# Optimization experiments

Measured on AMD Instinct MI355X. Metric: run time of the kernel, lower is better.

Reference implementation:

```python
import jax, jax.numpy as jnp
import numpy as np

B, N, DIM = 2, 2048, 1024
HEADS, DH, NUM_MEM = 8, 64, 4
EPS = 1e-5


def layer_norm(x, gamma):
    mu = x.mean(-1, keepdims=True)
    var = ((x - mu) ** 2).mean(-1, keepdims=True)
    return (x - mu) * jax.lax.rsqrt(var + EPS) * gamma


def setup_inputs() -> dict:
    key = jax.random.key(0)
    ks = jax.random.split(key, 7)
    x = jax.random.normal(ks[0], (B, N, DIM), jnp.float32)
    mask = jax.random.randint(ks[1], (B, N), 0, 2) > 0
    attn_bias = jax.random.normal(ks[2], (HEADS, N, N), jnp.float32) * 0.02
    gamma = jnp.ones((DIM,), jnp.float32)
    Wq = jax.random.normal(ks[3], (DIM, HEADS * DH), jnp.float32) * (DIM ** -0.5)
    Wkv = jax.random.normal(ks[4], (DIM, 2 * DH), jnp.float32) * (DIM ** -0.5)
    mem_kv = jax.random.normal(ks[5], (2, NUM_MEM, DH), jnp.float32)
    Wout = jax.random.normal(ks[6], (HEADS * DH, DIM), jnp.float32) * ((HEADS * DH) ** -0.5)
    return dict(x=x, attn_bias=attn_bias, gamma=gamma, Wq=Wq, Wkv=Wkv,
                mem_kv=mem_kv, Wout=Wout, mask=mask)


def reference(x, attn_bias, gamma, Wq, Wkv, mem_kv, Wout, mask):
    b, n, _ = x.shape
    # norm applied to query path only; kv comes from pre-norm x (self-attention)
    xn = layer_norm(x, gamma)
    q = (xn @ Wq).reshape(b, n, HEADS, DH).transpose(0, 2, 1, 3) * (DH ** -0.5)  # b h n d
    kv = x @ Wkv  # multi-query: single shared kv head
    k, v = kv[..., :DH], kv[..., DH:]
    mk = jnp.broadcast_to(mem_kv[0], (b, NUM_MEM, DH))
    mv = jnp.broadcast_to(mem_kv[1], (b, NUM_MEM, DH))
    k = jnp.concatenate([mk, k], axis=1)  # b (m+n) d
    v = jnp.concatenate([mv, v], axis=1)
    j = n + NUM_MEM
    bias = jnp.pad(attn_bias, ((0, 0), (0, 0), (NUM_MEM, 0)))  # zero bias on mem tokens
    maskp = jnp.pad(mask, ((0, 0), (NUM_MEM, 0)), constant_values=True)
    sim = jnp.einsum('bhid,bjd->bhij', q, k) + bias
    neg = -jnp.finfo(sim.dtype).max
    sim = jnp.where(maskp[:, None, None, :], sim, neg)
    causal = jnp.triu(jnp.ones((n, j), bool), k=NUM_MEM + 1)  # mem tokens always visible
    sim = jnp.where(causal, neg, sim)
    attn = jax.nn.softmax(sim, axis=-1)
    out = jnp.einsum('bhij,bjd->bhid', attn, v)
    out = out.transpose(0, 2, 1, 3).reshape(b, n, HEADS * DH)
    return out @ Wout
```

## Files before the change

kernel.cpp:

```cpp
#include <hip/hip_runtime.h>
#include <hip/hip_bf16.h>
#include <float.h>

#define B_ 2
#define N_ 2048
#define DIM_ 1024
#define HEADS_ 8
#define DH_ 64
#define NUM_MEM_ 4
#define ROWS_ (B_ * N_)
#define QCOLS_ (HEADS_ * DH_)
#define JTOT_ (N_ + NUM_MEM_)
#define JPAD_ 2176
#define CHUNKS_PER_BH_ 77

typedef __attribute__((ext_vector_type(8))) short short8v;
typedef __attribute__((ext_vector_type(4))) float f32x4;

static __device__ __forceinline__ ushort f2b(float f) {
    __hip_bfloat16 hb = __float2bfloat16(f);
    return *(ushort*)&hb;
}
static __device__ __forceinline__ uint pk2(float a, float b) {
    return ((uint)f2b(b) << 16) | (uint)f2b(a);
}
static __device__ __forceinline__ float b2f_lo(uint u) {
    union { uint x; float f; } c; c.x = u << 16; return c.f;
}
static __device__ __forceinline__ float b2f_hi(uint u) {
    union { uint x; float f; } c; c.x = u & 0xffff0000u; return c.f;
}

static __device__ __forceinline__ void wtrans_body(const float* __restrict__ W,
                                                   ushort* __restrict__ Wt,
                                                   int K, int N, int t) {
    int n = t % N;
    int k0 = (t / N) * 8;
    ushort u[8];
    #pragma unroll
    for (int j = 0; j < 8; ++j) u[j] = f2b(W[(size_t)(k0 + j) * N + n]);
    *(int4*)(Wt + (size_t)n * K + k0) = *(int4*)u;
}

__global__ __launch_bounds__(256) void ln_prep_kernel(const float* __restrict__ x,
                                                      const float* __restrict__ gamma,
                                                      const float* __restrict__ Wq,
                                                      const float* __restrict__ Wkv,
                                                      const float* __restrict__ Wout,
                                                      const float* __restrict__ mem_kv,
                                                      const int* __restrict__ mask,
                                                      ushort* __restrict__ xb,
                                                      ushort* __restrict__ xnb,
                                                      ushort* __restrict__ Wqt,
                                                      ushort* __restrict__ Wkvt,
                                                      ushort* __restrict__ Woutt,
                                                      ushort* __restrict__ Kb,
                                                      ushort* __restrict__ Vt,
                                                      ushort* __restrict__ amask) {
    int bid0 = blockIdx.x;
    if (bid0 < ROWS_) {
        int row = bid0;
        const float4 v = ((const float4*)(x + (size_t)row * DIM_))[threadIdx.x];
        float s  = v.x + v.y + v.z + v.w;
        float s2 = v.x * v.x + v.y * v.y + v.z * v.z + v.w * v.w;
        #pragma unroll
        for (int off = 32; off > 0; off >>= 1) {
            s  += __shfl_down(s, off);
            s2 += __shfl_down(s2, off);
        }
        __shared__ float ws1[4], ws2[4];
        int lane = threadIdx.x & 63, wid = threadIdx.x >> 6;
        if (lane == 0) { ws1[wid] = s; ws2[wid] = s2; }
        __syncthreads();
        float tot  = ws1[0] + ws1[1] + ws1[2] + ws1[3];
        float tot2 = ws2[0] + ws2[1] + ws2[2] + ws2[3];
        float mu  = tot * (1.0f / DIM_);
        float var = tot2 * (1.0f / DIM_) - mu * mu;
        float rs  = rsqrtf(var + 1e-5f);
        const float4 g = ((const float4*)gamma)[threadIdx.x];
        float vv[4] = {v.x, v.y, v.z, v.w};
        float gg[4] = {g.x, g.y, g.z, g.w};
        ushort xo[4], xno[4];
        #pragma unroll
        for (int j = 0; j < 4; ++j) {
            xo[j]  = f2b(vv[j]);
            xno[j] = f2b((vv[j] - mu) * rs * gg[j]);
        }
        *(int2*)(xb  + (size_t)row * DIM_ + threadIdx.x * 4) = *(int2*)xo;
        *(int2*)(xnb + (size_t)row * DIM_ + threadIdx.x * 4) = *(int2*)xno;
        return;
    }
    int bid = bid0 - ROWS_;
    int tid = threadIdx.x;
    if (bid < 256) {
        wtrans_body(Wq, Wqt, DIM_, QCOLS_, bid * 256 + tid);
    } else if (bid < 320) {
        wtrans_body(Wkv, Wkvt, DIM_, 2 * DH_, (bid - 256) * 256 + tid);
    } else if (bid < 576) {
        wtrans_body(Wout, Woutt, QCOLS_, DIM_, (bid - 320) * 256 + tid);
    } else if (bid < 640) {
        int t = (bid - 576) * 256 + tid;
        int d  = t & 63;
        int ji = (t >> 6) & 127;
        int b  = t >> 13;
        int j  = (ji < NUM_MEM_) ? ji : (2048 + ji);
        float kv_ = 0.f, vv = 0.f;
        if (ji < NUM_MEM_) {
            kv_ = mem_kv[ji * DH_ + d];
            vv  = mem_kv[NUM_MEM_ * DH_ + ji * DH_ + d];
        }
        Kb[((size_t)(b * JPAD_) + j) * DH_ + d] = f2b(kv_);
        Vt[((size_t)(b * DH_) + d) * JPAD_ + j] = f2b(vv);
    } else {
        int t = (bid - 640) * 256 + tid;
        if (t < B_ * JPAD_) {
            int b = t / JPAD_;
            int j = t % JPAD_;
            float v;
            if (j < NUM_MEM_) v = 0.f;
            else if (j < JTOT_) v = mask[b * N_ + (j - NUM_MEM_)] ? 0.f : -1e30f;
            else v = -1e30f;
            amask[(size_t)b * JPAD_ + j] = f2b(v);
        }
    }
}

template<int MODE>
static __device__ __forceinline__ void gemm64_body(ushort (*As)[40], ushort (*Bs)[40],
                                                   const ushort* __restrict__ A,
                                                   const ushort* __restrict__ Bt,
                                                   void* __restrict__ C,
                                                   void* __restrict__ C2,
                                                   int N, int K, int bx, int by) {
    int tid = threadIdx.x;
    int w = tid >> 6, l = tid & 63, lg = l >> 4, ll = l & 15;
    int r0 = by * 64, c0 = bx * 64;

    int arow = tid >> 2;
    int achk = (tid & 3) * 8;
    const ushort* Ap = A + (size_t)(r0 + arow) * K + achk;
    const ushort* Bp = Bt + (size_t)(c0 + arow) * K + achk;

    int4 a0 = *(const int4*)Ap;
    int4 b0 = *(const int4*)Bp;

    f32x4 acc[4] = {};

    int nk = K / 32;
    for (int ks = 0; ks < nk; ++ks) {
        __syncthreads();
        *(int4*)&As[arow][achk] = a0;
        *(int4*)&Bs[arow][achk] = b0;
        __syncthreads();
        int kn = (ks + 1 < nk) ? (ks + 1) * 32 : 0;
        a0 = *(const int4*)(Ap + kn);
        b0 = *(const int4*)(Bp + kn);
        short8v af, bf[4];
        af = *(const short8v*)&As[w * 16 + ll][lg * 8];
        #pragma unroll
        for (int ct = 0; ct < 4; ++ct)
            bf[ct] = *(const short8v*)&Bs[ct * 16 + ll][lg * 8];
        __builtin_amdgcn_s_setprio(1);
        #pragma unroll
        for (int ct = 0; ct < 4; ++ct)
            acc[ct] = __builtin_amdgcn_mfma_f32_16x16x32_bf16(af, bf[ct], acc[ct], 0, 0, 0);
        __builtin_amdgcn_s_setprio(0);
    }

    #pragma unroll
    for (int ct = 0; ct < 4; ++ct) {
        #pragma unroll
        for (int r = 0; r < 4; ++r) {
            int row = r0 + w * 16 + lg * 4 + r;
            int col = c0 + ct * 16 + ll;
            float val = acc[ct][r];
            if (MODE == 0) {
                ((ushort*)C)[(size_t)row * QCOLS_ + col] = f2b(val * 0.125f);
            } else {
                int b = row >> 11;
                int j = (row & 2047) + NUM_MEM_;
                if (col < DH_)
                    ((ushort*)C)[((size_t)(b * JPAD_) + j) * DH_ + col] = f2b(val);
                else
                    ((ushort*)C2)[((size_t)(b * DH_) + (col - DH_)) * JPAD_ + j] = f2b(val);
            }
        }
    }
}

__global__ __launch_bounds__(256) void gemm01_kernel(const ushort* __restrict__ xnb,
                                                     const ushort* __restrict__ Wqt,
                                                     ushort* __restrict__ qb,
                                                     const ushort* __restrict__ xb,
                                                     const ushort* __restrict__ Wkvt,
                                                     ushort* __restrict__ Kb,
                                                     ushort* __restrict__ Vt) {
    __shared__ ushort As[64][40];
    __shared__ ushort Bs[64][40];
    int bid = blockIdx.x;
    if (bid < 512) {
        gemm64_body<0>(As, Bs, xnb, Wqt, qb, nullptr, QCOLS_, DIM_, bid & 7, bid >> 3);
    } else {
        int r = bid - 512;
        gemm64_body<1>(As, Bs, xb, Wkvt, Kb, Vt, 2 * DH_, DIM_, r & 1, r >> 1);
    }
}

__global__ __launch_bounds__(256) void gemm_out_kernel(const ushort* __restrict__ A,
                                                       const ushort* __restrict__ Bt,
                                                       float* __restrict__ C,
                                                       int M, int N, int K) {
    __shared__ ushort As[128][40];
    __shared__ ushort Bs[64][40];
    int tid = threadIdx.x;
    int w = tid >> 6, l = tid & 63, lg = l >> 4, ll = l & 15;
    int r0 = blockIdx.y * 128, c0 = blockIdx.x * 64;

    int arow = tid >> 2;
    int achk = (tid & 3) * 8;
    const ushort* Ap  = A + (size_t)(r0 + arow) * K + achk;
    const ushort* Ap2 = Ap + (size_t)64 * K;
    const ushort* Bp  = Bt + (size_t)(c0 + arow) * K + achk;

    int4 a0 = *(const int4*)Ap;
    int4 a1 = *(const int4*)Ap2;
    int4 b0 = *(const int4*)Bp;

    f32x4 acc[2][4] = {};

    int nk = K / 32;
    for (int ks = 0; ks < nk; ++ks) {
        __syncthreads();
        *(int4*)&As[arow][achk]      = a0;
        *(int4*)&As[arow + 64][achk] = a1;
        *(int4*)&Bs[arow][achk]      = b0;
        __syncthreads();
        int kn = (ks + 1 < nk) ? (ks + 1) * 32 : 0;
        a0 = *(const int4*)(Ap + kn);
        a1 = *(const int4*)(Ap2 + kn);
        b0 = *(const int4*)(Bp + kn);
        short8v af[2], bf[4];
        af[0] = *(const short8v*)&As[w * 32 + ll][lg * 8];
        af[1] = *(const short8v*)&As[w * 32 + 16 + ll][lg * 8];
        #pragma unroll
        for (int ct = 0; ct < 4; ++ct)
            bf[ct] = *(const short8v*)&Bs[ct * 16 + ll][lg * 8];
        __builtin_amdgcn_s_setprio(1);
        #pragma unroll
        for (int rt = 0; rt < 2; ++rt)
            #pragma unroll
            for (int ct = 0; ct < 4; ++ct)
                acc[rt][ct] = __builtin_amdgcn_mfma_f32_16x16x32_bf16(af[rt], bf[ct], acc[rt][ct], 0, 0, 0);
        __builtin_amdgcn_s_setprio(0);
    }

    #pragma unroll
    for (int rt = 0; rt < 2; ++rt)
        #pragma unroll
        for (int ct = 0; ct < 4; ++ct)
            #pragma unroll
            for (int r = 0; r < 4; ++r) {
                int row = r0 + w * 32 + rt * 16 + lg * 4 + r;
                int col = c0 + ct * 16 + ll;
                C[(size_t)row * DIM_ + col] = acc[rt][ct][r];
            }
}

__global__ __launch_bounds__(256, 4) void fattn_split_kernel(const ushort* __restrict__ qb,
                                                             const ushort* __restrict__ Kb,
                                                             const ushort* __restrict__ Vt,
                                                             const float* __restrict__ bias,
                                                             const ushort* __restrict__ amask,
                                                             ushort* __restrict__ part_O,
                                                             float* __restrict__ part_ml) {
    __shared__ ushort Ks[64][72];
    __shared__ ushort Vs[64][72];
    __shared__ ushort Bb[64][68];

    int cid = blockIdx.x;
    int bh  = cid / CHUNKS_PER_BH_;
    int rem = cid - bh * CHUNKS_PER_BH_;
    int b = bh >> 3, h = bh & 7;
    int qt = 0, ci = 0;
    {
        int cum = 0;
        #pragma unroll 1
        for (int t = 0; t < 32; ++t) {
            int c = (t + 10) / 9;
            if (rem < cum + c) { qt = t; ci = rem - cum; break; }
            cum += c;
        }
    }
    int nt = qt + 2;
    int nc = (qt + 10) / 9;
    int t0 = ci * nt / nc;
    int t1 = (ci + 1) * nt / nc;
    int q0 = qt * 64;

    int tid = threadIdx.x;
    int w  = tid >> 6;
    int l  = tid & 63;
    int lg = l >> 4;
    int ll = l & 15;
    int i_row = q0 + w * 16 + ll;

    short8v aq0, aq1;
    {
        const ushort* qp = qb + ((size_t)(b * N_ + i_row)) * QCOLS_ + h * DH_;
        aq0 = *(const short8v*)(qp + lg * 8);
        aq1 = *(const short8v*)(qp + 32 + lg * 8);
    }

    int trow = tid >> 5;
    int tpc  = tid & 31;
    const float*  bias_rb = bias + ((size_t)h * N_ + q0 + trow) * N_;
    const ushort* am_row  = amask + (size_t)b * JPAD_;

    int sr = tid >> 3, sc = (tid & 7) * 8;
    const ushort* KbB = Kb + (size_t)b * JPAD_ * DH_;
    const ushort* VtB = Vt + (size_t)b * DH_ * JPAD_;

    int srcA = ((l & 16) << 1) + ll;
    int srcB = srcA + 16;
    bool hi = (l & 32) != 0;

    int jp0 = t0 * 64;
    int4 kr0 = *(const int4*)(KbB + (size_t)(jp0 + sr) * DH_ + sc);
    int4 kr1 = *(const int4*)(KbB + (size_t)(jp0 + sr + 32) * DH_ + sc);
    int4 vr0 = *(const int4*)(VtB + (size_t)sr * JPAD_ + jp0 + sc);
    int4 vr1 = *(const int4*)(VtB + (size_t)(sr + 32) * JPAD_ + jp0 + sc);

    uint bbc[8];
    {
        int j_e = jp0 + 2 * tpc;
        int sj  = j_e - NUM_MEM_;
        int sjc = sj < 0 ? 0 : (sj > N_ - 2 ? N_ - 2 : sj);
        uint am2 = *(const uint*)(am_row + j_e);
        float amf0 = b2f_lo(am2), amf1 = b2f_hi(am2);
        #pragma unroll
        for (int p = 0; p < 8; ++p) {
            float2 bv = *(const float2*)(bias_rb + (size_t)(8 * p) * N_ + sjc);
            int i_s = q0 + trow + 8 * p;
            float v0 = (j_e     < NUM_MEM_) ? 0.f : bv.x + amf0;
            float v1 = (j_e + 1 < NUM_MEM_) ? 0.f : bv.y + amf1;
            v0 = (j_e     <= i_s + NUM_MEM_) ? v0 : -1e30f;
            v1 = (j_e + 1 <= i_s + NUM_MEM_) ? v1 : -1e30f;
            bbc[p] = pk2(v0, v1);
        }
    }

    f32x4 oacc[4] = {};
    float mrow1 = -1e30f, lsum1 = 0.f;

    for (int jt = t0; jt < t1; ++jt) {
        __syncthreads();
        *(int4*)&Ks[sr][sc]      = kr0;
        *(int4*)&Ks[sr + 32][sc] = kr1;
        *(int4*)&Vs[sr][sc]      = vr0;
        *(int4*)&Vs[sr + 32][sc] = vr1;
        #pragma unroll
        for (int p = 0; p < 8; ++p)
            *(uint*)&Bb[trow + 8 * p][2 * tpc] = bbc[p];
        __syncthreads();

        int jn0 = (jt + 1 < t1 ? jt + 1 : jt) * 64;
        kr0 = *(const int4*)(KbB + (size_t)(jn0 + sr) * DH_ + sc);
        kr1 = *(const int4*)(KbB + (size_t)(jn0 + sr + 32) * DH_ + sc);
        vr0 = *(const int4*)(VtB + (size_t)sr * JPAD_ + jn0 + sc);
        vr1 = *(const int4*)(VtB + (size_t)(sr + 32) * JPAD_ + jn0 + sc);
        int j_e = jn0 + 2 * tpc;
        int sj  = j_e - NUM_MEM_;
        int sjc = sj < 0 ? 0 : (sj > N_ - 2 ? N_ - 2 : sj);
        uint am2n = *(const uint*)(am_row + j_e);
        float2 bvn[8];
        #pragma unroll
        for (int p = 0; p < 8; ++p)
            bvn[p] = *(const float2*)(bias_rb + (size_t)(8 * p) * N_ + sjc);

        float s[4][4];
        #pragma unroll
        for (int ct = 0; ct < 4; ++ct) {
            f32x4 acc = {};
            short8v bk0 = *(const short8v*)&Ks[ct * 16 + ll][lg * 8];
            short8v bk1 = *(const short8v*)&Ks[ct * 16 + ll][32 + lg * 8];
            __builtin_amdgcn_s_setprio(1);
            acc = __builtin_amdgcn_mfma_f32_16x16x32_bf16(bk0, aq0, acc, 0, 0, 0);
            acc = __builtin_amdgcn_mfma_f32_16x16x32_bf16(bk1, aq1, acc, 0, 0, 0);
            __builtin_amdgcn_s_setprio(0);
            uint2 ub = *(const uint2*)&Bb[w * 16 + ll][ct * 16 + lg * 4];
            s[ct][0] = acc[0] + b2f_lo(ub.x);
            s[ct][1] = acc[1] + b2f_hi(ub.x);
            s[ct][2] = acc[2] + b2f_lo(ub.y);
            s[ct][3] = acc[3] + b2f_hi(ub.y);
        }

        float m01 = fmaxf(fmaxf(s[0][0], s[0][1]), fmaxf(s[0][2], s[0][3]));
        float m23 = fmaxf(fmaxf(s[1][0], s[1][1]), fmaxf(s[1][2], s[1][3]));
        float m45 = fmaxf(fmaxf(s[2][0], s[2][1]), fmaxf(s[2][2], s[2][3]));
        float m67 = fmaxf(fmaxf(s[3][0], s[3][1]), fmaxf(s[3][2], s[3][3]));
        float m = fmaxf(fmaxf(m01, m23), fmaxf(m45, m67));
        m = fmaxf(m, __shfl_xor(m, 16));
        m = fmaxf(m, __shfl_xor(m, 32));
        float mn = fmaxf(mrow1, m);
        float scl = __expf(mrow1 - mn);
        mrow1 = mn;

        float ps = 0.f;
        #pragma unroll
        for (int ct = 0; ct < 4; ++ct)
            #pragma unroll
            for (int r = 0; r < 4; ++r) {
                float p = __expf(s[ct][r] - mn);
                s[ct][r] = p;
                ps += p;
            }
        ps += __shfl_xor(ps, 16);
        ps += __shfl_xor(ps, 32);
        lsum1 = lsum1 * scl + ps;

        uint pux[4], puy[4];
        #pragma unroll
        for (int ct = 0; ct < 4; ++ct) {
            pux[ct] = pk2(s[ct][0], s[ct][1]);
            puy[ct] = pk2(s[ct][2], s[ct][3]);
        }
        #pragma unroll
        for (int dt = 0; dt < 4; ++dt)
            #pragma unroll
            for (int r = 0; r < 4; ++r) oacc[dt][r] *= scl;

        #pragma unroll
        for (int c = 0; c < 2; ++c) {
            int cl = 2 * c, ch = 2 * c + 1;
            uint xA_l = (uint)__shfl((int)pux[cl], srcA);
            uint xA_h = (uint)__shfl((int)pux[ch], srcA);
            uint yA_l = (uint)__shfl((int)puy[cl], srcA);
            uint yA_h = (uint)__shfl((int)puy[ch], srcA);
            uint xB_l = (uint)__shfl((int)pux[cl], srcB);
            uint xB_h = (uint)__shfl((int)pux[ch], srcB);
            uint yB_l = (uint)__shfl((int)puy[cl], srcB);
            uint yB_h = (uint)__shfl((int)puy[ch], srcB);
            uint uu[4];
            uu[0] = hi ? xA_h : xA_l;
            uu[1] = hi ? yA_h : yA_l;
            uu[2] = hi ? xB_h : xB_l;
            uu[3] = hi ? yB_h : yB_l;
            short8v ptf = *(const short8v*)uu;
            __builtin_amdgcn_s_setprio(1);
            #pragma unroll
            for (int dt = 0; dt < 4; ++dt) {
                short8v bv = *(const short8v*)&Vs[dt * 16 + ll][c * 32 + lg * 8];
                oacc[dt] = __builtin_amdgcn_mfma_f32_16x16x32_bf16(bv, ptf, oacc[dt], 0, 0, 0);
            }
            __builtin_amdgcn_s_setprio(0);
        }

        {
            float amf0 = b2f_lo(am2n), amf1 = b2f_hi(am2n);
            #pragma unroll
            for (int p = 0; p < 8; ++p) {
                int i_s = q0 + trow + 8 * p;
                float v0 = (j_e     < NUM_MEM_) ? 0.f : bvn[p].x + amf0;
                float v1 = (j_e + 1 < NUM_MEM_) ? 0.f : bvn[p].y + amf1;
                v0 = (j_e     <= i_s + NUM_MEM_) ? v0 : -1e30f;
                v1 = (j_e + 1 <= i_s + NUM_MEM_) ? v1 : -1e30f;
                bbc[p] = pk2(v0, v1);
            }
        }
    }

    int slot = (bh * 32 + qt) * 4 + ci;
    ushort* po = part_O + (size_t)slot * 4096;
    #pragma unroll
    for (int dt = 0; dt < 4; ++dt) {
        uint2 pu;
        pu.x = pk2(oacc[dt][0], oacc[dt][1]);
        pu.y = pk2(oacc[dt][2], oacc[dt][3]);
        *(uint2*)&po[(w * 16 + ll) * 64 + dt * 16 + lg * 4] = pu;
    }
    if (lg == 0) {
        part_ml[(size_t)slot * 128 + (w * 16 + ll) * 2]     = mrow1;
        part_ml[(size_t)slot * 128 + (w * 16 + ll) * 2 + 1] = lsum1;
    }
}

__global__ __launch_bounds__(256) void merge_kernel(const ushort* __restrict__ part_O,
                                                    const float* __restrict__ part_ml,
                                                    ushort* __restrict__ attn_ob) {
    int bid = blockIdx.x;
    int qt = bid & 31;
    int bh = bid >> 5;
    int b = bh >> 3, h = bh & 7;
    int nc = (qt + 10) / 9;
    int tid = threadIdx.x;
    int row = tid >> 2;
    int dseg = (tid & 3) * 16;
    int slot0 = bid * 4;

    float M = -1e30f;
    #pragma unroll
    for (int c = 0; c < 4; ++c) {
        if (c >= nc) break;
        M = fmaxf(M, part_ml[(size_t)(slot0 + c) * 128 + row * 2]);
    }
    float den = 0.f;
    float num[16] = {};
    #pragma unroll
    for (int c = 0; c < 4; ++c) {
        if (c >= nc) break;
        float m_c = part_ml[(size_t)(slot0 + c) * 128 + row * 2];
        float l_c = part_ml[(size_t)(slot0 + c) * 128 + row * 2 + 1];
        float wgt = __expf(m_c - M);
        den += wgt * l_c;
        const uint4* src = (const uint4*)(part_O + (size_t)(slot0 + c) * 4096 + row * 64 + dseg);
        uint4 v0 = src[0];
        uint4 v1 = src[1];
        uint uu[8] = { v0.x, v0.y, v0.z, v0.w, v1.x, v1.y, v1.z, v1.w };
        #pragma unroll
        for (int e = 0; e < 8; ++e) {
            num[e * 2 + 0] += wgt * b2f_lo(uu[e]);
            num[e * 2 + 1] += wgt * b2f_hi(uu[e]);
        }
    }
    float inv = 1.f / den;
    ushort o[16];
    #pragma unroll
    for (int e = 0; e < 16; ++e) o[e] = f2b(num[e] * inv);
    int i = qt * 64 + row;
    ushort* dst = attn_ob + ((size_t)(b * N_ + i)) * QCOLS_ + h * DH_ + dseg;
    *(int4*)dst = *(int4*)o;
    *(int4*)(dst + 8) = *(int4*)(o + 8);
}

extern "C" void kernel_launch(void* const* d_in, const int* in_sizes, int n_in,
                              void* d_out, int out_size, void* d_ws, size_t ws_size,
                              hipStream_t stream) {
    const float* x         = (const float*)d_in[0];
    const float* attn_bias = (const float*)d_in[1];
    const float* gamma     = (const float*)d_in[2];
    const float* Wq        = (const float*)d_in[3];
    const float* Wkv       = (const float*)d_in[4];
    const float* mem_kv    = (const float*)d_in[5];
    const float* Wout      = (const float*)d_in[6];
    const int*   mask      = (const int*)d_in[7];
    float* out = (float*)d_out;

    char* wsb = (char*)d_ws;
    ushort* xb      = (ushort*)wsb;
    ushort* xnb     = (ushort*)(wsb + (8u  << 20));
    ushort* qb      = (ushort*)(wsb + (16u << 20));
    ushort* attn_ob = (ushort*)(wsb + (20u << 20));
    ushort* Kb      = (ushort*)(wsb + (24u << 20));
    ushort* Vt      = (ushort*)(wsb + (25u << 20));
    ushort* Wqt     = (ushort*)(wsb + (26u << 20));
    ushort* Wkvt    = (ushort*)(wsb + (27u << 20));
    ushort* Woutt   = (ushort*)(wsb + (28u << 20));
    ushort* amask   = (ushort*)(wsb + (29u << 20));
    ushort* part_O  = (ushort*)(wsb + (32u << 20));
    float*  part_ml = (float*)(wsb + (64u << 20));

    ln_prep_kernel<<<ROWS_ + 657, 256, 0, stream>>>(x, gamma, Wq, Wkv, Wout, mem_kv, mask,
                                                    xb, xnb, Wqt, Wkvt, Woutt, Kb, Vt, amask);
    gemm01_kernel<<<640, 256, 0, stream>>>(xnb, Wqt, qb, xb, Wkvt, Kb, Vt);
    fattn_split_kernel<<<16 * CHUNKS_PER_BH_, 256, 0, stream>>>(qb, Kb, Vt, attn_bias, amask, part_O, part_ml);
    merge_kernel<<<512, 256, 0, stream>>>(part_O, part_ml, attn_ob);
    gemm_out_kernel<<<dim3(DIM_ / 64, ROWS_ / 128), 256, 0, stream>>>(attn_ob, Woutt, out, ROWS_, DIM_, QCOLS_);
}
```

Measured before the change: 94.89 us.

## Deepen GEMM K-tiles to 64, write single-chunk attention directly, reorder blocks

Both projection GEMMs now stage 64-wide K slices per iteration instead of 32. This halves the number of barrier-separated loop steps and issues two MFMAs per fragment, at the cost of more shared memory and registers. The attention kernel now normalizes and writes the output directly for query tiles that have only one chunk, and the merge kernel skips those tiles. This removes partial-buffer traffic for them. The attention block index is also interleaved by batch so that blocks sharing the same bias head run close together.

```diff
diff --git a/kernel.cpp b/kernel.cpp
--- a/kernel.cpp
+++ b/kernel.cpp
@@ -126,7 +126,7 @@
 }
 
 template<int MODE>
-static __device__ __forceinline__ void gemm64_body(ushort (*As)[40], ushort (*Bs)[40],
+static __device__ __forceinline__ void gemm64_body(ushort (*As)[72], ushort (*Bs)[72],
                                                    const ushort* __restrict__ A,
                                                    const ushort* __restrict__ Bt,
                                                    void* __restrict__ C,
@@ -136,34 +136,47 @@
     int w = tid >> 6, l = tid & 63, lg = l >> 4, ll = l & 15;
     int r0 = by * 64, c0 = bx * 64;
 
-    int arow = tid >> 2;
-    int achk = (tid & 3) * 8;
-    const ushort* Ap = A + (size_t)(r0 + arow) * K + achk;
-    const ushort* Bp = Bt + (size_t)(c0 + arow) * K + achk;
-
-    int4 a0 = *(const int4*)Ap;
-    int4 b0 = *(const int4*)Bp;
+    int sr = tid >> 3;
+    int sc = (tid & 7) * 8;
+    const ushort* Ap0 = A + (size_t)(r0 + sr) * K + sc;
+    const ushort* Ap1 = A + (size_t)(r0 + sr + 32) * K + sc;
+    const ushort* Bp0 = Bt + (size_t)(c0 + sr) * K + sc;
+    const ushort* Bp1 = Bt + (size_t)(c0 + sr + 32) * K + sc;
+
+    int4 a0 = *(const int4*)Ap0;
+    int4 a1 = *(const int4*)Ap1;
+    int4 b0 = *(const int4*)Bp0;
+    int4 b1 = *(const int4*)Bp1;
 
     f32x4 acc[4] = {};
 
-    int nk = K / 32;
+    int nk = K / 64;
     for (int ks = 0; ks < nk; ++ks) {
         __syncthreads();
-        *(int4*)&As[arow][achk] = a0;
-        *(int4*)&Bs[arow][achk] = b0;
+        *(int4*)&As[sr][sc]      = a0;
+        *(int4*)&As[sr + 32][sc] = a1;
+        *(int4*)&Bs[sr][sc]      = b0;
+        *(int4*)&Bs[sr + 32][sc] = b1;
         __syncthreads();
-        int kn = (ks + 1 < nk) ? (ks + 1) * 32 : 0;
-        a0 = *(const int4*)(Ap + kn);
-        b0 = *(const int4*)(Bp + kn);
-        short8v af, bf[4];
-        af = *(const short8v*)&As[w * 16 + ll][lg * 8];
-        #pragma unroll
-        for (int ct = 0; ct < 4; ++ct)
-            bf[ct] = *(const short8v*)&Bs[ct * 16 + ll][lg * 8];
+        int kn = (ks + 1 < nk) ? (ks + 1) * 64 : 0;
+        a0 = *(const int4*)(Ap0 + kn);
+        a1 = *(const int4*)(Ap1 + kn);
+        b0 = *(const int4*)(Bp0 + kn);
+        b1 = *(const int4*)(Bp1 + kn);
+        short8v af0 = *(const short8v*)&As[w * 16 + ll][lg * 8];
+        short8v af1 = *(const short8v*)&As[w * 16 + ll][32 + lg * 8];
+        short8v bf0[4], bf1[4];
+        #pragma unroll
+        for (int ct = 0; ct < 4; ++ct) {
+            bf0[ct] = *(const short8v*)&Bs[ct * 16 + ll][lg * 8];
+            bf1[ct] = *(const short8v*)&Bs[ct * 16 + ll][32 + lg * 8];
+        }
         __builtin_amdgcn_s_setprio(1);
         #pragma unroll
-        for (int ct = 0; ct < 4; ++ct)
-            acc[ct] = __builtin_amdgcn_mfma_f32_16x16x32_bf16(af, bf[ct], acc[ct], 0, 0, 0);
+        for (int ct = 0; ct < 4; ++ct) {
+            acc[ct] = __builtin_amdgcn_mfma_f32_16x16x32_bf16(af0, bf0[ct], acc[ct], 0, 0, 0);
+            acc[ct] = __builtin_amdgcn_mfma_f32_16x16x32_bf16(af1, bf1[ct], acc[ct], 0, 0, 0);
+        }
         __builtin_amdgcn_s_setprio(0);
     }
 
@@ -195,8 +208,8 @@
                                                      const ushort* __restrict__ Wkvt,
                                                      ushort* __restrict__ Kb,
                                                      ushort* __restrict__ Vt) {
-    __shared__ ushort As[64][40];
-    __shared__ ushort Bs[64][40];
+    __shared__ ushort As[64][72];
+    __shared__ ushort Bs[64][72];
     int bid = blockIdx.x;
     if (bid < 512) {
         gemm64_body<0>(As, Bs, xnb, Wqt, qb, nullptr, QCOLS_, DIM_, bid & 7, bid >> 3);
@@ -210,47 +223,60 @@
                                                        const ushort* __restrict__ Bt,
                                                        float* __restrict__ C,
                                                        int M, int N, int K) {
-    __shared__ ushort As[128][40];
-    __shared__ ushort Bs[64][40];
+    __shared__ ushort As[128][72];
+    __shared__ ushort Bs[64][72];
     int tid = threadIdx.x;
     int w = tid >> 6, l = tid & 63, lg = l >> 4, ll = l & 15;
     int r0 = blockIdx.y * 128, c0 = blockIdx.x * 64;
 
-    int arow = tid >> 2;
-    int achk = (tid & 3) * 8;
-    const ushort* Ap  = A + (size_t)(r0 + arow) * K + achk;
-    const ushort* Ap2 = Ap + (size_t)64 * K;
-    const ushort* Bp  = Bt + (size_t)(c0 + arow) * K + achk;
-
-    int4 a0 = *(const int4*)Ap;
-    int4 a1 = *(const int4*)Ap2;
-    int4 b0 = *(const int4*)Bp;
+    int sr = tid >> 3;
+    int sc = (tid & 7) * 8;
+    const ushort* Ap[4];
+    #pragma unroll
+    for (int p = 0; p < 4; ++p) Ap[p] = A + (size_t)(r0 + sr + 32 * p) * K + sc;
+    const ushort* Bp0 = Bt + (size_t)(c0 + sr) * K + sc;
+    const ushort* Bp1 = Bt + (size_t)(c0 + sr + 32) * K + sc;
+
+    int4 ar[4];
+    #pragma unroll
+    for (int p = 0; p < 4; ++p) ar[p] = *(const int4*)Ap[p];
+    int4 b0 = *(const int4*)Bp0;
+    int4 b1 = *(const int4*)Bp1;
 
     f32x4 acc[2][4] = {};
 
-    int nk = K / 32;
+    int nk = K / 64;
     for (int ks = 0; ks < nk; ++ks) {
         __syncthreads();
-        *(int4*)&As[arow][achk]      = a0;
-        *(int4*)&As[arow + 64][achk] = a1;
-        *(int4*)&Bs[arow][achk]      = b0;
+        #pragma unroll
+        for (int p = 0; p < 4; ++p) *(int4*)&As[sr + 32 * p][sc] = ar[p];
+        *(int4*)&Bs[sr][sc]      = b0;
+        *(int4*)&Bs[sr + 32][sc] = b1;
         __syncthreads();
-        int kn = (ks + 1 < nk) ? (ks + 1) * 32 : 0;
-        a0 = *(const int4*)(Ap + kn);
-        a1 = *(const int4*)(Ap2 + kn);
-        b0 = *(const int4*)(Bp + kn);
-        short8v af[2], bf[4];
-        af[0] = *(const short8v*)&As[w * 32 + ll][lg * 8];
-        af[1] = *(const short8v*)&As[w * 32 + 16 + ll][lg * 8];
-        #pragma unroll
-        for (int ct = 0; ct < 4; ++ct)
-            bf[ct] = *(const short8v*)&Bs[ct * 16 + ll][lg * 8];
+        int kn = (ks + 1 < nk) ? (ks + 1) * 64 : 0;
+        #pragma unroll
+        for (int p = 0; p < 4; ++p) ar[p] = *(const int4*)(Ap[p] + kn);
+        b0 = *(const int4*)(Bp0 + kn);
+        b1 = *(const int4*)(Bp1 + kn);
+        short8v af[2][2], bf[4][2];
+        #pragma unroll
+        for (int rt = 0; rt < 2; ++rt) {
+            af[rt][0] = *(const short8v*)&As[w * 32 + rt * 16 + ll][lg * 8];
+            af[rt][1] = *(const short8v*)&As[w * 32 + rt * 16 + ll][32 + lg * 8];
+        }
+        #pragma unroll
+        for (int ct = 0; ct < 4; ++ct) {
+            bf[ct][0] = *(const short8v*)&Bs[ct * 16 + ll][lg * 8];
+            bf[ct][1] = *(const short8v*)&Bs[ct * 16 + ll][32 + lg * 8];
+        }
         __builtin_amdgcn_s_setprio(1);
         #pragma unroll
         for (int rt = 0; rt < 2; ++rt)
             #pragma unroll
-            for (int ct = 0; ct < 4; ++ct)
-                acc[rt][ct] = __builtin_amdgcn_mfma_f32_16x16x32_bf16(af[rt], bf[ct], acc[rt][ct], 0, 0, 0);
+            for (int ct = 0; ct < 4; ++ct) {
+                acc[rt][ct] = __builtin_amdgcn_mfma_f32_16x16x32_bf16(af[rt][0], bf[ct][0], acc[rt][ct], 0, 0, 0);
+                acc[rt][ct] = __builtin_amdgcn_mfma_f32_16x16x32_bf16(af[rt][1], bf[ct][1], acc[rt][ct], 0, 0, 0);
+            }
         __builtin_amdgcn_s_setprio(0);
     }
 
@@ -272,15 +298,18 @@
                                                              const float* __restrict__ bias,
                                                              const ushort* __restrict__ amask,
                                                              ushort* __restrict__ part_O,
-                                                             float* __restrict__ part_ml) {
+                                                             float* __restrict__ part_ml,
+                                                             ushort* __restrict__ attn_ob) {
     __shared__ ushort Ks[64][72];
     __shared__ ushort Vs[64][72];
     __shared__ ushort Bb[64][68];
 
     int cid = blockIdx.x;
-    int bh  = cid / CHUNKS_PER_BH_;
-    int rem = cid - bh * CHUNKS_PER_BH_;
-    int b = bh >> 3, h = bh & 7;
+    int b    = cid & 1;
+    int rest = cid >> 1;
+    int h    = rest / CHUNKS_PER_BH_;
+    int rem  = rest - h * CHUNKS_PER_BH_;
+    int bh   = b * 8 + h;
     int qt = 0, ci = 0;
     {
         int cum = 0;
@@ -469,18 +498,30 @@
         }
     }
 
-    int slot = (bh * 32 + qt) * 4 + ci;
-    ushort* po = part_O + (size_t)slot * 4096;
-    #pragma unroll
-    for (int dt = 0; dt < 4; ++dt) {
-        uint2 pu;
-        pu.x = pk2(oacc[dt][0], oacc[dt][1]);
-        pu.y = pk2(oacc[dt][2], oacc[dt][3]);
-        *(uint2*)&po[(w * 16 + ll) * 64 + dt * 16 + lg * 4] = pu;
-    }
-    if (lg == 0) {
-        part_ml[(size_t)slot * 128 + (w * 16 + ll) * 2]     = mrow1;
-        part_ml[(size_t)slot * 128 + (w * 16 + ll) * 2 + 1] = lsum1;
+    if (nc == 1) {
+        float inv = 1.f / lsum1;
+        ushort* dst = attn_ob + ((size_t)(b * N_ + i_row)) * QCOLS_ + h * DH_;
+        #pragma unroll
+        for (int dt = 0; dt < 4; ++dt) {
+            uint2 pu;
+            pu.x = pk2(oacc[dt][0] * inv, oacc[dt][1] * inv);
+            pu.y = pk2(oacc[dt][2] * inv, oacc[dt][3] * inv);
+            *(uint2*)(dst + dt * 16 + lg * 4) = pu;
+        }
+    } else {
+        int slot = (bh * 32 + qt) * 4 + ci;
+        ushort* po = part_O + (size_t)slot * 4096;
+        #pragma unroll
+        for (int dt = 0; dt < 4; ++dt) {
+            uint2 pu;
+            pu.x = pk2(oacc[dt][0], oacc[dt][1]);
+            pu.y = pk2(oacc[dt][2], oacc[dt][3]);
+            *(uint2*)&po[(w * 16 + ll) * 64 + dt * 16 + lg * 4] = pu;
+        }
+        if (lg == 0) {
+            part_ml[(size_t)slot * 128 + (w * 16 + ll) * 2]     = mrow1;
+            part_ml[(size_t)slot * 128 + (w * 16 + ll) * 2 + 1] = lsum1;
+        }
     }
 }
 
@@ -489,9 +530,10 @@
                                                     ushort* __restrict__ attn_ob) {
     int bid = blockIdx.x;
     int qt = bid & 31;
+    int nc = (qt + 10) / 9;
+    if (nc < 2) return;
     int bh = bid >> 5;
     int b = bh >> 3, h = bh & 7;
-    int nc = (qt + 10) / 9;
     int tid = threadIdx.x;
     int row = tid >> 2;
     int dseg = (tid & 3) * 16;
@@ -562,7 +604,8 @@
     ln_prep_kernel<<<ROWS_ + 657, 256, 0, stream>>>(x, gamma, Wq, Wkv, Wout, mem_kv, mask,
                                                     xb, xnb, Wqt, Wkvt, Woutt, Kb, Vt, amask);
     gemm01_kernel<<<640, 256, 0, stream>>>(xnb, Wqt, qb, xb, Wkvt, Kb, Vt);
-    fattn_split_kernel<<<16 * CHUNKS_PER_BH_, 256, 0, stream>>>(qb, Kb, Vt, attn_bias, amask, part_O, part_ml);
+    fattn_split_kernel<<<16 * CHUNKS_PER_BH_, 256, 0, stream>>>(qb, Kb, Vt, attn_bias, amask,
+                                                                part_O, part_ml, attn_ob);
     merge_kernel<<<512, 256, 0, stream>>>(part_O, part_ml, attn_ob);
     gemm_out_kernel<<<dim3(DIM_ / 64, ROWS_ / 128), 256, 0, stream>>>(attn_ob, Woutt, out, ROWS_, DIM_, QCOLS_);
 }
```

Result: slower. 104.6 us (+10.3%).
